# Kernel tuning notes

Measured on AMD Instinct MI355X. Metric: run time of the kernel, lower is better.

Reference implementation:

```python
import jax, jax.numpy as jnp
import numpy as np

N_NODES = 50000


def gcn_conv(x, W, b, src, dst, n):
    # PyG GCNConv: linear transform, add self-loops, symmetric normalization,
    # scatter-add aggregation from src -> dst, then bias.
    h = x @ W  # [N, out]
    loop = jnp.arange(n, dtype=src.dtype)
    s = jnp.concatenate([src, loop])
    d = jnp.concatenate([dst, loop])
    deg = jax.ops.segment_sum(jnp.ones(s.shape[0], dtype=h.dtype), d, num_segments=n)
    dinv = jnp.where(deg > 0, jax.lax.rsqrt(deg), 0.0)
    norm = dinv[s] * dinv[d]  # [E+N]
    msg = h[s] * norm[:, None]
    out = jax.ops.segment_sum(msg, d, num_segments=n)
    return out + b


def setup_inputs() -> dict:
    key = jax.random.key(0)
    ks = jax.random.split(key, 10)
    F_in, H, C = 256, 128, 128
    E, EL = 320000, 200000
    x = jax.random.normal(ks[0], (N_NODES, F_in), dtype=jnp.float32)
    edge_index = jax.random.randint(ks[1], (2, E), 0, N_NODES, dtype=jnp.int32)
    edge_label_index = jax.random.randint(ks[2], (2, EL), 0, N_NODES, dtype=jnp.int32)
    def glorot(k, shape):
        lim = np.sqrt(6.0 / (shape[0] + shape[1]))
        return jax.random.uniform(k, shape, jnp.float32, -lim, lim)
    W0 = glorot(ks[3], (F_in, H))
    b0 = jnp.zeros((H,), jnp.float32)
    W1 = glorot(ks[4], (H, H))
    b1 = jnp.zeros((H,), jnp.float32)
    W2 = glorot(ks[5], (H, C))
    b2 = jnp.zeros((C,), jnp.float32)
    return {"x": x, "edge_index": edge_index, "edge_label_index": edge_label_index,
            "W0": W0, "b0": b0, "W1": W1, "b1": b1, "W2": W2, "b2": b2}


def reference(x, edge_index, edge_label_index, W0, b0, W1, b1, W2, b2):
    src, dst = edge_index[0], edge_index[1]
    n = x.shape[0]
    # drop_edge keep_ratio == 1.0 -> all edges kept (deterministic)
    h = jax.nn.relu(gcn_conv(x, W0, b0, src, dst, n))
    h = jax.nn.relu(gcn_conv(h, W1, b1, src, dst, n))
    z = gcn_conv(h, W2, b2, src, dst, n)  # final conv, no activation
    # decode: dot product over candidate edge pairs
    eli = edge_label_index.astype(jnp.int32)
    logits = jnp.sum(z[eli[0]] * z[eli[1]], axis=-1)  # [E_label]
    return logits
```

## Files before the change

### kernel.cpp

```cpp
#include <hip/hip_runtime.h>
#include <hip/hip_bf16.h>


typedef __attribute__((ext_vector_type(8))) short short8v;
typedef __attribute__((ext_vector_type(4))) short short4v;
typedef __attribute__((ext_vector_type(4))) float f32x4;

__device__ inline unsigned bf16_rne(float f) {
    unsigned u = __float_as_uint(f);
    return (u + 0x7FFF + ((u >> 16) & 1)) >> 16;
}


__global__ void count_deg_kernel(const int* __restrict__ dst, int* __restrict__ deg, int E) {
    int e = blockIdx.x * blockDim.x + threadIdx.x;
    if (e < E) atomicAdd(&deg[dst[e]], 1);
}

__global__ __launch_bounds__(1024) void scan1_kernel(int* __restrict__ data,
                                                     int* __restrict__ sums, int n) {
    __shared__ int tmp[1024];
    int t = threadIdx.x;
    int idx = blockIdx.x * 1024 + t;
    int val = (idx < n) ? data[idx] : 0;
    tmp[t] = val;
    __syncthreads();
#pragma unroll
    for (int off = 1; off < 1024; off <<= 1) {
        int v = (t >= off) ? tmp[t - off] : 0;
        __syncthreads();
        tmp[t] += v;
        __syncthreads();
    }
    if (idx < n) data[idx] = tmp[t] - val;
    if (t == 1023) sums[blockIdx.x] = tmp[t];
}

__global__ void scan2_kernel(int* __restrict__ sums, int nb) {
    int lane = threadIdx.x & 63;
    int v = (lane < nb) ? sums[lane] : 0;
    int orig = v;
#pragma unroll
    for (int d = 1; d < 64; d <<= 1) {
        int t2 = __shfl_up(v, d, 64);
        if (lane >= d) v += t2;
    }
    if (lane < nb) sums[lane] = v - orig;
}

__global__ __launch_bounds__(1024) void scan3_kernel(int* __restrict__ data,
                                                     const int* __restrict__ sums, int n) {
    int idx = blockIdx.x * 1024 + threadIdx.x;
    if (idx < n && blockIdx.x > 0) data[idx] += sums[blockIdx.x];
}

__global__ void make_dinv_kernel(const int* __restrict__ off, float* __restrict__ dinv,
                                 int n, int E) {
    int v = blockIdx.x * blockDim.x + threadIdx.x;
    if (v < n) {
        int o1 = (v + 1 < n) ? off[v + 1] : E;
        float d = (float)(o1 - off[v]) + 1.0f;
        dinv[v] = 1.0f / sqrtf(d);
    }
}

__global__ void csr_fill_kernel(const int* __restrict__ src, const int* __restrict__ dst,
                                const int* __restrict__ off, int* __restrict__ fill,
                                int* __restrict__ csr_src, int E) {
    int e = blockIdx.x * blockDim.x + threadIdx.x;
    if (e >= E) return;
    int d = dst[e];
    int pos = atomicAdd(&fill[d], 1);
    csr_src[off[d] + pos] = src[e];
}


__global__ void split_w_kernel(const float* __restrict__ W, short* __restrict__ Wh,
                               short* __restrict__ Wl, int K) {
    int idx = blockIdx.x * blockDim.x + threadIdx.x;
    if (idx >= K * 128) return;
    int k = idx >> 7, col = idx & 127;
    float f = W[idx];
    unsigned h = bf16_rne(f);
    float fh = __uint_as_float(h << 16);
    unsigned l = bf16_rne(f - fh);
    Wh[col * K + k] = (short)h;
    Wl[col * K + k] = (short)l;
}


#define SWZ(row, kbyte) (((row) * 128) + ((kbyte) ^ (((row) & 7) << 4)))

__global__ __launch_bounds__(256) void gemm_mfma_kernel(const float* __restrict__ A,
                                                        const short* __restrict__ Wh_g,
                                                        const short* __restrict__ Wl_g,
                                                        const float* __restrict__ dinv,
                                                        float* __restrict__ out,
                                                        int M, int K) {
    __shared__ __align__(16) char smem[65536];
    char* Ah = smem;
    char* Al = smem + 16384;
    char* Bh = smem + 32768;
    char* Bl = smem + 49152;

    const int t = threadIdx.x;
    const int lane = t & 63;
    const int w = t >> 6;
    const int block_row = blockIdx.x * 128;

    f32x4 acc[2][8];
#pragma unroll
    for (int m = 0; m < 2; ++m)
#pragma unroll
        for (int c = 0; c < 8; ++c) acc[m][c] = (f32x4){0.f, 0.f, 0.f, 0.f};

    for (int k0 = 0; k0 < K; k0 += 64) {
        __syncthreads();

#pragma unroll
        for (int i = 0; i < 8; ++i) {
            int idx = t + i * 256;
            int row = idx >> 4;
            int kq  = (idx & 15) << 2;
            int grow = block_row + row;
            float4 v = make_float4(0.f, 0.f, 0.f, 0.f);
            if (grow < M) v = *reinterpret_cast<const float4*>(&A[(size_t)grow * K + k0 + kq]);
            short4v hv, lv;
            float f[4] = {v.x, v.y, v.z, v.w};
#pragma unroll
            for (int j = 0; j < 4; ++j) {
                unsigned h = bf16_rne(f[j]);
                float fh = __uint_as_float(h << 16);
                unsigned l = bf16_rne(f[j] - fh);
                hv[j] = (short)h;
                lv[j] = (short)l;
            }
            int off = SWZ(row, kq * 2);
            *reinterpret_cast<short4v*>(&Ah[off]) = hv;
            *reinterpret_cast<short4v*>(&Al[off]) = lv;
        }
#pragma unroll
        for (int i = 0; i < 4; ++i) {
            int idx = t + i * 256;
            int row = idx >> 3;
            int u   = idx & 7;
            size_t g = (size_t)row * K + k0 + u * 8;
            short8v hv = *reinterpret_cast<const short8v*>(&Wh_g[g]);
            short8v lv = *reinterpret_cast<const short8v*>(&Wl_g[g]);
            int off = SWZ(row, u * 16);
            *reinterpret_cast<short8v*>(&Bh[off]) = hv;
            *reinterpret_cast<short8v*>(&Bl[off]) = lv;
        }
        __syncthreads();

        short8v ah[2][2], al[2][2];
#pragma unroll
        for (int m = 0; m < 2; ++m)
#pragma unroll
            for (int ks = 0; ks < 2; ++ks) {
                int row = w * 32 + m * 16 + (lane & 15);
                int kb  = ks * 64 + (lane >> 4) * 16;
                ah[m][ks] = *reinterpret_cast<const short8v*>(&Ah[SWZ(row, kb)]);
                al[m][ks] = *reinterpret_cast<const short8v*>(&Al[SWZ(row, kb)]);
            }

#pragma unroll
        for (int c = 0; c < 8; ++c) {
            short8v bh[2], bl[2];
#pragma unroll
            for (int ks = 0; ks < 2; ++ks) {
                int rb = c * 16 + (lane & 15);
                int kb = ks * 64 + (lane >> 4) * 16;
                bh[ks] = *reinterpret_cast<const short8v*>(&Bh[SWZ(rb, kb)]);
                bl[ks] = *reinterpret_cast<const short8v*>(&Bl[SWZ(rb, kb)]);
            }
#pragma unroll
            for (int m = 0; m < 2; ++m)
#pragma unroll
                for (int ks = 0; ks < 2; ++ks) {
                    acc[m][c] = __builtin_amdgcn_mfma_f32_16x16x32_bf16(ah[m][ks], bh[ks], acc[m][c], 0, 0, 0);
                    acc[m][c] = __builtin_amdgcn_mfma_f32_16x16x32_bf16(ah[m][ks], bl[ks], acc[m][c], 0, 0, 0);
                    acc[m][c] = __builtin_amdgcn_mfma_f32_16x16x32_bf16(al[m][ks], bh[ks], acc[m][c], 0, 0, 0);
                }
        }
    }

#pragma unroll
    for (int m = 0; m < 2; ++m)
#pragma unroll
        for (int r = 0; r < 4; ++r) {
            int row = block_row + w * 32 + m * 16 + (lane >> 4) * 4 + r;
            float ds = (row < M) ? dinv[row] : 0.0f;
#pragma unroll
            for (int c = 0; c < 8; ++c) {
                int col = c * 16 + (lane & 15);
                if (row < M) out[(size_t)row * 128 + col] = acc[m][c][r] * ds;
            }
        }
}


__global__ __launch_bounds__(256) void gather_kernel(const int* __restrict__ off,
                                                     const int* __restrict__ csr_src,
                                                     const float* __restrict__ dinv,
                                                     const float* __restrict__ hp,
                                                     const float* __restrict__ bias,
                                                     float* __restrict__ out,
                                                     int n, int E, int do_relu) {
    int gid = blockIdx.x * blockDim.x + threadIdx.x;
    int v = gid >> 6;
    int lane = gid & 63;
    if (v >= n) return;

    int o0 = off[v];
    int o1 = (v + 1 < n) ? off[v + 1] : E;

    const float2* __restrict__ hp2 = reinterpret_cast<const float2*>(hp);
    float2 sv = hp2[(size_t)v * 64 + lane];
    float ax = sv.x, ay = sv.y;
    float bx = 0.0f, by = 0.0f;

    for (int base = o0; base < o1; base += 64) {
        int cnt = min(64, o1 - base);
        int myidx = (lane < cnt) ? csr_src[base + lane] : 0;
        int j = 0;
        for (; j + 4 <= cnt; j += 4) {
            int i0 = __shfl(myidx, j,     64);
            int i1 = __shfl(myidx, j + 1, 64);
            int i2 = __shfl(myidx, j + 2, 64);
            int i3 = __shfl(myidx, j + 3, 64);
            float2 h0 = hp2[(size_t)i0 * 64 + lane];
            float2 h1 = hp2[(size_t)i1 * 64 + lane];
            float2 h2 = hp2[(size_t)i2 * 64 + lane];
            float2 h3 = hp2[(size_t)i3 * 64 + lane];
            ax += h0.x; ay += h0.y;
            bx += h1.x; by += h1.y;
            ax += h2.x; ay += h2.y;
            bx += h3.x; by += h3.y;
        }
        for (; j < cnt; ++j) {
            int s = __shfl(myidx, j, 64);
            float2 hv = hp2[(size_t)s * 64 + lane];
            ax += hv.x; ay += hv.y;
        }
    }

    float dv = dinv[v];
    float2 bb = *reinterpret_cast<const float2*>(&bias[lane * 2]);
    float ox = dv * (ax + bx) + bb.x;
    float oy = dv * (ay + by) + bb.y;
    if (do_relu) { ox = fmaxf(ox, 0.0f); oy = fmaxf(oy, 0.0f); }
    *reinterpret_cast<float2*>(&out[(size_t)v * 128 + lane * 2]) = make_float2(ox, oy);
}


__global__ __launch_bounds__(256) void decode_kernel(const int* __restrict__ ia,
                                                     const int* __restrict__ ib,
                                                     const float* __restrict__ z,
                                                     float* __restrict__ out, int EL) {
    int gid = blockIdx.x * blockDim.x + threadIdx.x;
    int e = gid >> 6;
    int lane = gid & 63;
    if (e >= EL) return;
    int a = ia[e], b = ib[e];
    float2 za = *reinterpret_cast<const float2*>(&z[(size_t)a * 128 + lane * 2]);
    float2 zb = *reinterpret_cast<const float2*>(&z[(size_t)b * 128 + lane * 2]);
    float s = za.x * zb.x + za.y * zb.y;
#pragma unroll
    for (int off = 32; off > 0; off >>= 1) s += __shfl_down(s, off, 64);
    if (lane == 0) out[e] = s;
}


extern "C" void kernel_launch(void* const* d_in, const int* in_sizes, int n_in,
                              void* d_out, int out_size, void* d_ws, size_t ws_size,
                              hipStream_t stream) {
    const float* x   = (const float*)d_in[0];
    const int*   ei  = (const int*)d_in[1];
    const int*   eli = (const int*)d_in[2];
    const float* W0  = (const float*)d_in[3];
    const float* b0  = (const float*)d_in[4];
    const float* W1  = (const float*)d_in[5];
    const float* b1  = (const float*)d_in[6];
    const float* W2  = (const float*)d_in[7];
    const float* b2  = (const float*)d_in[8];
    float* out = (float*)d_out;

    const int H    = in_sizes[4];
    const int F_in = in_sizes[3] / H;
    const int n    = in_sizes[0] / F_in;
    const int E    = in_sizes[1] / 2;
    const int EL   = in_sizes[2] / 2;

    const int* src = ei;
    const int* dst = ei + E;
    const int* la  = eli;
    const int* lb  = eli + EL;

    char* ws = (char*)d_ws;
    size_t p = 0;
    auto alloc = [&](size_t bytes) { char* r = ws + p; p = (p + bytes + 255) & ~(size_t)255; return r; };
    float* dinv    = (float*)alloc((size_t)n * 4);
    int*   off     = (int*)  alloc((size_t)n * 4);
    int*   csr_src = (int*)  alloc((size_t)E * 4);
    int*   sums    = (int*)  alloc(64 * 4);
    short* W0h     = (short*)alloc((size_t)F_in * H * 2);
    short* W0l     = (short*)alloc((size_t)F_in * H * 2);
    short* W1h     = (short*)alloc((size_t)H * H * 2);
    short* W1l     = (short*)alloc((size_t)H * H * 2);
    short* W2h     = (short*)alloc((size_t)H * H * 2);
    short* W2l     = (short*)alloc((size_t)H * H * 2);
    float* bufA    = (float*)alloc((size_t)n * 128 * 4);
    float* bufB    = (float*)alloc((size_t)n * 128 * 4);
    int*   fill    = (int*)bufB;

    const int T = 256;
    dim3 blk(T);

    hipMemsetAsync(off, 0, (size_t)n * 4, stream);
    hipMemsetAsync(fill, 0, (size_t)n * 4, stream);
    split_w_kernel<<<(F_in * H + T - 1) / T, blk, 0, stream>>>(W0, W0h, W0l, F_in);
    split_w_kernel<<<(H * H + T - 1) / T, blk, 0, stream>>>(W1, W1h, W1l, H);
    split_w_kernel<<<(H * H + T - 1) / T, blk, 0, stream>>>(W2, W2h, W2l, H);
    count_deg_kernel<<<(E + T - 1) / T, blk, 0, stream>>>(dst, off, E);
    int nb = (n + 1023) / 1024;
    scan1_kernel<<<nb, 1024, 0, stream>>>(off, sums, n);
    scan2_kernel<<<1, 64, 0, stream>>>(sums, nb);
    scan3_kernel<<<nb, 1024, 0, stream>>>(off, sums, n);
    make_dinv_kernel<<<(n + T - 1) / T, blk, 0, stream>>>(off, dinv, n, E);
    csr_fill_kernel<<<(E + T - 1) / T, blk, 0, stream>>>(src, dst, off, fill, csr_src, E);

    const int mblocks       = (n + 127) / 128;
    const int gather_blocks = (int)(((long long)n * 64 + T - 1) / T);

    gemm_mfma_kernel<<<mblocks, blk, 0, stream>>>(x, W0h, W0l, dinv, bufA, n, F_in);
    gather_kernel<<<gather_blocks, blk, 0, stream>>>(off, csr_src, dinv, bufA, b0, bufB, n, E, 1);

    gemm_mfma_kernel<<<mblocks, blk, 0, stream>>>(bufB, W1h, W1l, dinv, bufA, n, H);
    gather_kernel<<<gather_blocks, blk, 0, stream>>>(off, csr_src, dinv, bufA, b1, bufB, n, E, 1);

    gemm_mfma_kernel<<<mblocks, blk, 0, stream>>>(bufB, W2h, W2l, dinv, bufA, n, H);
    gather_kernel<<<gather_blocks, blk, 0, stream>>>(off, csr_src, dinv, bufA, b2, bufB, n, E, 0);

    const int dec_blocks = (int)(((long long)EL * 64 + T - 1) / T);
    decode_kernel<<<dec_blocks, blk, 0, stream>>>(la, lb, bufB, out, EL);
}
```

Baseline: 342.7 us.

## Replace LDS-staged GEMM with direct-to-register MFMA loads; widen decode loads

The GEMM no longer stages A and W tiles through shared memory. Each wave loads its A fragment straight from global memory into registers, converts it to the bf16 hi/lo split there, and reads W fragments directly from global memory (relying on L1/L2 caching of the small weights). K becomes a template parameter, and the block tile shrinks from 128 to 64 rows to raise occupancy and drop the barriers. The decode kernel now uses 32 lanes per edge with float4 loads instead of 64 lanes with float2, which halves the shuffle steps and the thread count. The risk is that uncoalesced fragment-shaped global loads and repeated W reads from cache cost more than the LDS traffic they replace.

```diff
diff --git a/kernel.cpp b/kernel.cpp
--- a/kernel.cpp
+++ b/kernel.cpp
@@ -3,7 +3,6 @@
 
 
 typedef __attribute__((ext_vector_type(8))) short short8v;
-typedef __attribute__((ext_vector_type(4))) short short4v;
 typedef __attribute__((ext_vector_type(4))) float f32x4;
 
 __device__ inline unsigned bf16_rne(float f) {
@@ -89,114 +88,72 @@
 }
 
 
-#define SWZ(row, kbyte) (((row) * 128) + ((kbyte) ^ (((row) & 7) << 4)))
-
-__global__ __launch_bounds__(256) void gemm_mfma_kernel(const float* __restrict__ A,
-                                                        const short* __restrict__ Wh_g,
-                                                        const short* __restrict__ Wl_g,
+template<int K>
+__global__ __launch_bounds__(256) void gemm_mfma_direct(const float* __restrict__ A,
+                                                        const short* __restrict__ Wh,
+                                                        const short* __restrict__ Wl,
                                                         const float* __restrict__ dinv,
                                                         float* __restrict__ out,
-                                                        int M, int K) {
-    __shared__ __align__(16) char smem[65536];
-    char* Ah = smem;
-    char* Al = smem + 16384;
-    char* Bh = smem + 32768;
-    char* Bl = smem + 49152;
-
+                                                        int M) {
     const int t = threadIdx.x;
     const int lane = t & 63;
     const int w = t >> 6;
-    const int block_row = blockIdx.x * 128;
-
-    f32x4 acc[2][8];
-#pragma unroll
-    for (int m = 0; m < 2; ++m)
-#pragma unroll
-        for (int c = 0; c < 8; ++c) acc[m][c] = (f32x4){0.f, 0.f, 0.f, 0.f};
-
-    for (int k0 = 0; k0 < K; k0 += 64) {
-        __syncthreads();
-
-#pragma unroll
-        for (int i = 0; i < 8; ++i) {
-            int idx = t + i * 256;
-            int row = idx >> 4;
-            int kq  = (idx & 15) << 2;
-            int grow = block_row + row;
-            float4 v = make_float4(0.f, 0.f, 0.f, 0.f);
-            if (grow < M) v = *reinterpret_cast<const float4*>(&A[(size_t)grow * K + k0 + kq]);
-            short4v hv, lv;
-            float f[4] = {v.x, v.y, v.z, v.w};
-#pragma unroll
-            for (int j = 0; j < 4; ++j) {
+    const int row16 = blockIdx.x * 64 + w * 16;
+    const int arow = min(row16 + (lane & 15), M - 1);
+    const int kgrp = (lane >> 4) * 8;
+    const int bcol = lane & 15;
+
+    const float* Abase = A + (size_t)arow * K + kgrp;
+
+    f32x4 acc[8];
+#pragma unroll
+    for (int c = 0; c < 8; ++c) acc[c] = (f32x4){0.f, 0.f, 0.f, 0.f};
+
+#pragma unroll
+    for (int kt = 0; kt < K / 64; ++kt) {
+        short8v ah[2], al[2];
+#pragma unroll
+        for (int ks = 0; ks < 2; ++ks) {
+            const float* ap = Abase + kt * 64 + ks * 32;
+            float4 v0 = *reinterpret_cast<const float4*>(ap);
+            float4 v1 = *reinterpret_cast<const float4*>(ap + 4);
+            float f[8] = {v0.x, v0.y, v0.z, v0.w, v1.x, v1.y, v1.z, v1.w};
+#pragma unroll
+            for (int j = 0; j < 8; ++j) {
                 unsigned h = bf16_rne(f[j]);
                 float fh = __uint_as_float(h << 16);
                 unsigned l = bf16_rne(f[j] - fh);
-                hv[j] = (short)h;
-                lv[j] = (short)l;
+                ah[ks][j] = (short)h;
+                al[ks][j] = (short)l;
             }
-            int off = SWZ(row, kq * 2);
-            *reinterpret_cast<short4v*>(&Ah[off]) = hv;
-            *reinterpret_cast<short4v*>(&Al[off]) = lv;
-        }
-#pragma unroll
-        for (int i = 0; i < 4; ++i) {
-            int idx = t + i * 256;
-            int row = idx >> 3;
-            int u   = idx & 7;
-            size_t g = (size_t)row * K + k0 + u * 8;
-            short8v hv = *reinterpret_cast<const short8v*>(&Wh_g[g]);
-            short8v lv = *reinterpret_cast<const short8v*>(&Wl_g[g]);
-            int off = SWZ(row, u * 16);
-            *reinterpret_cast<short8v*>(&Bh[off]) = hv;
-            *reinterpret_cast<short8v*>(&Bl[off]) = lv;
-        }
-        __syncthreads();
-
-        short8v ah[2][2], al[2][2];
-#pragma unroll
-        for (int m = 0; m < 2; ++m)
-#pragma unroll
-            for (int ks = 0; ks < 2; ++ks) {
-                int row = w * 32 + m * 16 + (lane & 15);
-                int kb  = ks * 64 + (lane >> 4) * 16;
-                ah[m][ks] = *reinterpret_cast<const short8v*>(&Ah[SWZ(row, kb)]);
-                al[m][ks] = *reinterpret_cast<const short8v*>(&Al[SWZ(row, kb)]);
-            }
-
+        }
 #pragma unroll
         for (int c = 0; c < 8; ++c) {
-            short8v bh[2], bl[2];
-#pragma unroll
-            for (int ks = 0; ks < 2; ++ks) {
-                int rb = c * 16 + (lane & 15);
-                int kb = ks * 64 + (lane >> 4) * 16;
-                bh[ks] = *reinterpret_cast<const short8v*>(&Bh[SWZ(rb, kb)]);
-                bl[ks] = *reinterpret_cast<const short8v*>(&Bl[SWZ(rb, kb)]);
-            }
-#pragma unroll
-            for (int m = 0; m < 2; ++m)
-#pragma unroll
-                for (int ks = 0; ks < 2; ++ks) {
-                    acc[m][c] = __builtin_amdgcn_mfma_f32_16x16x32_bf16(ah[m][ks], bh[ks], acc[m][c], 0, 0, 0);
-                    acc[m][c] = __builtin_amdgcn_mfma_f32_16x16x32_bf16(ah[m][ks], bl[ks], acc[m][c], 0, 0, 0);
-                    acc[m][c] = __builtin_amdgcn_mfma_f32_16x16x32_bf16(al[m][ks], bh[ks], acc[m][c], 0, 0, 0);
-                }
-        }
-    }
-
-#pragma unroll
-    for (int m = 0; m < 2; ++m)
-#pragma unroll
-        for (int r = 0; r < 4; ++r) {
-            int row = block_row + w * 32 + m * 16 + (lane >> 4) * 4 + r;
-            float ds = (row < M) ? dinv[row] : 0.0f;
-#pragma unroll
-            for (int c = 0; c < 8; ++c) {
-                int col = c * 16 + (lane & 15);
-                if (row < M) out[(size_t)row * 128 + col] = acc[m][c][r] * ds;
-            }
-        }
+            const short* bh_p = Wh + (size_t)(c * 16 + bcol) * K + kt * 64 + kgrp;
+            const short* bl_p = Wl + (size_t)(c * 16 + bcol) * K + kt * 64 + kgrp;
+            short8v bh0 = *reinterpret_cast<const short8v*>(bh_p);
+            short8v bh1 = *reinterpret_cast<const short8v*>(bh_p + 32);
+            short8v bl0 = *reinterpret_cast<const short8v*>(bl_p);
+            short8v bl1 = *reinterpret_cast<const short8v*>(bl_p + 32);
+            acc[c] = __builtin_amdgcn_mfma_f32_16x16x32_bf16(ah[0], bh0, acc[c], 0, 0, 0);
+            acc[c] = __builtin_amdgcn_mfma_f32_16x16x32_bf16(ah[0], bl0, acc[c], 0, 0, 0);
+            acc[c] = __builtin_amdgcn_mfma_f32_16x16x32_bf16(al[0], bh0, acc[c], 0, 0, 0);
+            acc[c] = __builtin_amdgcn_mfma_f32_16x16x32_bf16(ah[1], bh1, acc[c], 0, 0, 0);
+            acc[c] = __builtin_amdgcn_mfma_f32_16x16x32_bf16(ah[1], bl1, acc[c], 0, 0, 0);
+            acc[c] = __builtin_amdgcn_mfma_f32_16x16x32_bf16(al[1], bh1, acc[c], 0, 0, 0);
+        }
+    }
+
+#pragma unroll
+    for (int r = 0; r < 4; ++r) {
+        int row = row16 + (lane >> 4) * 4 + r;
+        if (row < M) {
+            float ds = dinv[row];
+#pragma unroll
+            for (int c = 0; c < 8; ++c)
+                out[(size_t)row * 128 + c * 16 + bcol] = acc[c][r] * ds;
+        }
+    }
 }
 
 
@@ -259,16 +216,17 @@
                                                      const float* __restrict__ z,
                                                      float* __restrict__ out, int EL) {
     int gid = blockIdx.x * blockDim.x + threadIdx.x;
-    int e = gid >> 6;
-    int lane = gid & 63;
+    int e = gid >> 5;
+    int l5 = gid & 31;
     if (e >= EL) return;
     int a = ia[e], b = ib[e];
-    float2 za = *reinterpret_cast<const float2*>(&z[(size_t)a * 128 + lane * 2]);
-    float2 zb = *reinterpret_cast<const float2*>(&z[(size_t)b * 128 + lane * 2]);
-    float s = za.x * zb.x + za.y * zb.y;
-#pragma unroll
-    for (int off = 32; off > 0; off >>= 1) s += __shfl_down(s, off, 64);
-    if (lane == 0) out[e] = s;
+    const float4* z4 = reinterpret_cast<const float4*>(z);
+    float4 za = z4[(size_t)a * 32 + l5];
+    float4 zb = z4[(size_t)b * 32 + l5];
+    float s = za.x * zb.x + za.y * zb.y + za.z * zb.z + za.w * zb.w;
+#pragma unroll
+    for (int off = 16; off > 0; off >>= 1) s += __shfl_down(s, off, 64);
+    if (l5 == 0) out[e] = s;
 }
 
 
@@ -330,18 +288,18 @@
     make_dinv_kernel<<<(n + T - 1) / T, blk, 0, stream>>>(off, dinv, n, E);
     csr_fill_kernel<<<(E + T - 1) / T, blk, 0, stream>>>(src, dst, off, fill, csr_src, E);
 
-    const int mblocks       = (n + 127) / 128;
+    const int mblocks       = (n + 63) / 64;
     const int gather_blocks = (int)(((long long)n * 64 + T - 1) / T);
 
-    gemm_mfma_kernel<<<mblocks, blk, 0, stream>>>(x, W0h, W0l, dinv, bufA, n, F_in);
+    gemm_mfma_direct<256><<<mblocks, blk, 0, stream>>>(x, W0h, W0l, dinv, bufA, n);
     gather_kernel<<<gather_blocks, blk, 0, stream>>>(off, csr_src, dinv, bufA, b0, bufB, n, E, 1);
 
-    gemm_mfma_kernel<<<mblocks, blk, 0, stream>>>(bufB, W1h, W1l, dinv, bufA, n, H);
+    gemm_mfma_direct<128><<<mblocks, blk, 0, stream>>>(bufB, W1h, W1l, dinv, bufA, n);
     gather_kernel<<<gather_blocks, blk, 0, stream>>>(off, csr_src, dinv, bufA, b1, bufB, n, E, 1);
 
-    gemm_mfma_kernel<<<mblocks, blk, 0, stream>>>(bufB, W2h, W2l, dinv, bufA, n, H);
+    gemm_mfma_direct<128><<<mblocks, blk, 0, stream>>>(bufB, W2h, W2l, dinv, bufA, n);
     gather_kernel<<<gather_blocks, blk, 0, stream>>>(off, csr_src, dinv, bufA, b2, bufB, n, E, 0);
 
-    const int dec_blocks = (int)(((long long)EL * 64 + T - 1) / T);
+    const int dec_blocks = (int)(((long long)EL * 32 + T - 1) / T);
     decode_kernel<<<dec_blocks, blk, 0, stream>>>(la, lb, bufB, out, EL);
 }
```

Measured after the change: 402.9 us. 17.6% more time.
